# Optimization experiments

Hardware: AMD Instinct MI355X
Metric: run time of the kernel (lower is better)

The kernel has to match this reference:

```python
import jax, jax.numpy as jnp
import numpy as np

EPS = 1e-05


def setup_inputs() -> dict:
    key = jax.random.key(0)
    kx, = jax.random.split(key, 1)
    B, C, T = 8, 512, 8192
    x = jax.random.normal(kx, (B, C, T), dtype=jnp.float32)
    weight = jnp.ones((1, C, 1), dtype=jnp.float32)
    bias = jnp.zeros((1, C, 1), dtype=jnp.float32)
    return {"x": x, "weight": weight, "bias": bias}


def reference(x, weight, bias):
    # x: [B, C, T]; causal (running) per-channel mean/var over time.
    T = x.shape[-1]
    count = jnp.arange(1, T + 1, dtype=x.dtype)  # [T], broadcasts over B,C
    cumsum = jnp.cumsum(x, axis=-1)
    cumsum_sq = jnp.cumsum(x * x, axis=-1)
    mean = cumsum / count
    var = cumsum_sq / count - mean * mean
    x_norm = (x - mean) * jax.lax.rsqrt(var + EPS)
    return x_norm * weight + bias
```

## Files before the change

### kernel.cpp

```cpp
#include <hip/hip_runtime.h>
#include <math.h>

#define EPS 1e-5f
#define T_LEN 8192

template<int CTRL, int RM>
__device__ __forceinline__ float dpp_add(float x) {
    int sh = __builtin_amdgcn_update_dpp(0, __float_as_int(x),
                                         CTRL, RM, 0xF, false);
    return x + __int_as_float(sh);
}

__device__ __forceinline__ float wave64_incl_scan(float x) {
    x = dpp_add<0x111, 0xF>(x);
    x = dpp_add<0x112, 0xF>(x);
    x = dpp_add<0x114, 0xF>(x);
    x = dpp_add<0x118, 0xF>(x);
    x = dpp_add<0x142, 0xA>(x);
    x = dpp_add<0x143, 0xC>(x);
    return x;
}

__global__ __launch_bounds__(1024, 8) void causal_ln_kernel(
    const float* __restrict__ x,
    const float* __restrict__ weight,
    const float* __restrict__ bias,
    float* __restrict__ out,
    int C)
{
    __shared__ float2 wtot[16];

    const int t    = threadIdx.x;
    const int lane = t & 63;
    const int wid  = t >> 6;
    const int row  = blockIdx.x;

    const float wv = weight[row % C];
    const float bv = bias[row % C];

    const float4* xg = (const float4*)(x + (long long)row * T_LEN);
    float4 v0 = xg[2 * t];
    float4 v1 = xg[2 * t + 1];

    float rcv[8];
#pragma unroll
    for (int i = 0; i < 8; ++i)
        rcv[i] = __builtin_amdgcn_rcpf((float)(8 * t + i + 1));

    float xs[8] = {v0.x, v0.y, v0.z, v0.w, v1.x, v1.y, v1.z, v1.w};

    float s = 0.f, s2 = 0.f;
#pragma unroll
    for (int i = 0; i < 8; ++i) { s += xs[i]; s2 += xs[i] * xs[i]; }

    float ws  = wave64_incl_scan(s);
    float ws2 = wave64_incl_scan(s2);

    if (lane == 63) wtot[wid] = make_float2(ws, ws2);
    __syncthreads();

    float off1 = 0.f, off2 = 0.f;
#pragma unroll
    for (int w = 0; w < 15; ++w) {
        if (w < wid) { off1 += wtot[w].x; off2 += wtot[w].y; }
    }

    float run  = off1 + (ws  - s);
    float run2 = off2 + (ws2 - s2);

#pragma unroll
    for (int i = 0; i < 8; ++i) {
        float xi = xs[i];
        run  += xi;
        run2 += xi * xi;
        float mean = run * rcv[i];
        float var  = fmaxf(run2 * rcv[i] - mean * mean, 0.f);
        float rinv = __builtin_amdgcn_rsqf(var + EPS);
        xs[i] = (xi - mean) * rinv * wv + bv;
    }

    float4* og = (float4*)(out + (long long)row * T_LEN);
    og[2 * t]     = make_float4(xs[0], xs[1], xs[2], xs[3]);
    og[2 * t + 1] = make_float4(xs[4], xs[5], xs[6], xs[7]);
}

extern "C" void kernel_launch(void* const* d_in, const int* in_sizes, int n_in,
                              void* d_out, int out_size, void* d_ws, size_t ws_size,
                              hipStream_t stream) {
    const float* x      = (const float*)d_in[0];
    const float* weight = (const float*)d_in[1];
    const float* bias   = (const float*)d_in[2];
    float* out          = (float*)d_out;

    const int C = in_sizes[1];
    const int T = 8192;
    const int rows = in_sizes[0] / T;

    dim3 grid(rows), block(1024);
    hipLaunchKernelGGL(causal_ln_kernel, grid, block, 0, stream,
                       x, weight, bias, out, C);
}
```

Measured before the change: 233.6 us.

## Split causal layernorm into prefix-sum pass and per-segment normalize pass

Replaces the single 1024-thread-per-row kernel with two kernels. The first computes per-512-element segment prefix sums of x and x^2 into workspace. The second normalizes each segment with one wave and no block-level barrier. This aims to raise parallelism and remove the block-wide sync in the main pass, at the cost of reading x twice and a second launch.

```diff
diff --git a/kernel.cpp b/kernel.cpp
--- a/kernel.cpp
+++ b/kernel.cpp
@@ -3,6 +3,8 @@
 
 #define EPS 1e-5f
 #define T_LEN 8192
+#define SEG 512
+#define SEGS_PER_ROW (T_LEN / SEG)
 
 template<int CTRL, int RM>
 __device__ __forceinline__ float dpp_add(float x) {
@@ -10,7 +12,6 @@
                                          CTRL, RM, 0xF, false);
     return x + __int_as_float(sh);
 }
-
 __device__ __forceinline__ float wave64_incl_scan(float x) {
     x = dpp_add<0x111, 0xF>(x);
     x = dpp_add<0x112, 0xF>(x);
@@ -20,34 +21,75 @@
     x = dpp_add<0x143, 0xC>(x);
     return x;
 }
+__device__ __forceinline__ float rd63(float x) {
+    return __int_as_float(__builtin_amdgcn_readlane(__float_as_int(x), 63));
+}
 
-__global__ __launch_bounds__(1024, 8) void causal_ln_kernel(
+__global__ __launch_bounds__(1024) void causal_ln_pass1(
     const float* __restrict__ x,
-    const float* __restrict__ weight,
-    const float* __restrict__ bias,
-    float* __restrict__ out,
-    int C)
+    float2* __restrict__ partial)
 {
-    __shared__ float2 wtot[16];
+    __shared__ float2 wtot[SEGS_PER_ROW];
 
     const int t    = threadIdx.x;
     const int lane = t & 63;
     const int wid  = t >> 6;
     const int row  = blockIdx.x;
 
-    const float wv = weight[row % C];
-    const float bv = bias[row % C];
+    const float4* xg = (const float4*)(x + (long long)row * T_LEN);
+    float4 a = xg[2 * t];
+    float4 b = xg[2 * t + 1];
 
-    const float4* xg = (const float4*)(x + (long long)row * T_LEN);
-    float4 v0 = xg[2 * t];
-    float4 v1 = xg[2 * t + 1];
+    float s  = a.x + a.y + a.z + a.w + b.x + b.y + b.z + b.w;
+    float s2 = a.x*a.x + a.y*a.y + a.z*a.z + a.w*a.w
+             + b.x*b.x + b.y*b.y + b.z*b.z + b.w*b.w;
 
+    float ts  = rd63(wave64_incl_scan(s));
+    float ts2 = rd63(wave64_incl_scan(s2));
+
+    if (lane == 0) wtot[wid] = make_float2(ts, ts2);
+    __syncthreads();
+
+    if (t < SEGS_PER_ROW) {
+        float p1 = 0.f, p2 = 0.f;
+#pragma unroll
+        for (int w = 0; w < SEGS_PER_ROW - 1; ++w) {
+            if (w < t) { p1 += wtot[w].x; p2 += wtot[w].y; }
+        }
+        partial[row * SEGS_PER_ROW + t] = make_float2(p1, p2);
+    }
+}
+
+__global__ __launch_bounds__(256) void causal_ln_pass2(
+    const float* __restrict__ x,
+    const float2* __restrict__ partial,
+    const float* __restrict__ weight,
+    const float* __restrict__ bias,
+    float* __restrict__ out,
+    int C)
+{
+    const int t    = threadIdx.x;
+    const int lane = t & 63;
+    const int wid  = t >> 6;
+    const int seg  = blockIdx.x * 4 + wid;
+    const int row  = seg >> 4;
+    const int w    = seg & (SEGS_PER_ROW - 1);
+
+    const float2 pre = partial[seg];
+    const float  wv  = weight[row % C];
+    const float  bv  = bias[row % C];
+
+    const float4* xg = (const float4*)(x + (long long)row * T_LEN + w * SEG);
+    float4 a = xg[2 * lane];
+    float4 b = xg[2 * lane + 1];
+
+    const float cb = (float)(w * SEG + lane * 8);
     float rcv[8];
 #pragma unroll
     for (int i = 0; i < 8; ++i)
-        rcv[i] = __builtin_amdgcn_rcpf((float)(8 * t + i + 1));
+        rcv[i] = __builtin_amdgcn_rcpf(cb + (float)(i + 1));
 
-    float xs[8] = {v0.x, v0.y, v0.z, v0.w, v1.x, v1.y, v1.z, v1.w};
+    float xs[8] = {a.x, a.y, a.z, a.w, b.x, b.y, b.z, b.w};
 
     float s = 0.f, s2 = 0.f;
 #pragma unroll
@@ -56,17 +98,8 @@
     float ws  = wave64_incl_scan(s);
     float ws2 = wave64_incl_scan(s2);
 
-    if (lane == 63) wtot[wid] = make_float2(ws, ws2);
-    __syncthreads();
-
-    float off1 = 0.f, off2 = 0.f;
-#pragma unroll
-    for (int w = 0; w < 15; ++w) {
-        if (w < wid) { off1 += wtot[w].x; off2 += wtot[w].y; }
-    }
-
-    float run  = off1 + (ws  - s);
-    float run2 = off2 + (ws2 - s2);
+    float run  = pre.x + (ws  - s);
+    float run2 = pre.y + (ws2 - s2);
 
 #pragma unroll
     for (int i = 0; i < 8; ++i) {
@@ -79,9 +112,9 @@
         xs[i] = (xi - mean) * rinv * wv + bv;
     }
 
-    float4* og = (float4*)(out + (long long)row * T_LEN);
-    og[2 * t]     = make_float4(xs[0], xs[1], xs[2], xs[3]);
-    og[2 * t + 1] = make_float4(xs[4], xs[5], xs[6], xs[7]);
+    float4* og = (float4*)(out + (long long)row * T_LEN + w * SEG);
+    og[2 * lane]     = make_float4(xs[0], xs[1], xs[2], xs[3]);
+    og[2 * lane + 1] = make_float4(xs[4], xs[5], xs[6], xs[7]);
 }
 
 extern "C" void kernel_launch(void* const* d_in, const int* in_sizes, int n_in,
@@ -96,7 +129,11 @@
     const int T = 8192;
     const int rows = in_sizes[0] / T;
 
-    dim3 grid(rows), block(1024);
-    hipLaunchKernelGGL(causal_ln_kernel, grid, block, 0, stream,
-                       x, weight, bias, out, C);
+    float2* partial = (float2*)d_ws;
+
+    hipLaunchKernelGGL(causal_ln_pass1, dim3(rows), dim3(1024), 0, stream,
+                       x, partial);
+    hipLaunchKernelGGL(causal_ln_pass2, dim3(rows * SEGS_PER_ROW / 4),
+                       dim3(256), 0, stream,
+                       x, partial, weight, bias, out, C);
 }
```

Measured after the change: 246.5 us. +5.5%, slower.
